# Kernel tuning notes

Measured on AMD Instinct MI355X. Metric: run time of the kernel, lower is better.

Reference implementation:

```python
import jax, jax.numpy as jnp
import numpy as np

# Topologies derived from init kwargs (inputs=64, outputs=64, state=512, net1 hidden=[512])
D = 64 + 64 + 512                      # 640 = concat(input, prev_output, state)
NET1 = [D, 512, 64]
NET3 = [D] + NET1 + [512]              # [640, 640, 512, 64, 512] (code reuses mutated net1 topo)
W_TOTAL = sum(NET3[j] * NET3[j + 1] for j in range(len(NET3) - 1))  # 802816
B_TOTAL = sum(NET3[1:])                # 1728
NET2 = [D] + NET1 + [W_TOTAL + B_TOTAL]  # [640, 640, 512, 64, 804544]


def _leaky(v):
    return jnp.where(v >= 0, v, 0.01 * v)


def setup_inputs() -> dict:
    key = jax.random.key(0)
    ks = jax.random.split(key, 16)
    inp = {
        "x": jax.random.normal(ks[0], (64,), jnp.float32),
        "prev_output": jnp.zeros((64,), jnp.float32),
        "state": jnp.zeros((512,), jnp.float32),
    }
    # net1 params (Linear stores W as [out, in])
    for i in range(len(NET1) - 1):
        inp[f"net1_w{i}"] = jax.random.normal(ks[1 + i], (NET1[i + 1], NET1[i]), jnp.float32) * 0.02
        inp[f"net1_b{i}"] = jnp.zeros((NET1[i + 1],), jnp.float32)
    # net2 params
    for i in range(len(NET2) - 1):
        inp[f"net2_w{i}"] = jax.random.normal(ks[5 + i], (NET2[i + 1], NET2[i]), jnp.float32) * 0.02
        inp[f"net2_b{i}"] = jnp.zeros((NET2[i + 1],), jnp.float32)
    return inp


def reference(x, prev_output, state,
              net1_w0, net1_b0, net1_w1, net1_b1,
              net2_w0, net2_b0, net2_w1, net2_b1,
              net2_w2, net2_b2, net2_w3, net2_b3):
    inpt = jnp.concatenate([x, prev_output, state])  # [640]

    # net2: hypernetwork producing flattened weights+biases for net3
    h = _leaky(net2_w0 @ inpt + net2_b0)
    h = _leaky(net2_w1 @ h + net2_b1)
    h = _leaky(net2_w2 @ h + net2_b2)
    x2 = jnp.tanh(net2_w3 @ h + net2_b3) * 0.5       # [W_TOTAL + B_TOTAL]
    weights = x2[:W_TOTAL]
    bias = x2[W_TOTAL:]

    # net3: apply generated weights sequentially (state update)
    x3 = inpt
    wi, bi = 0, 0
    for j in range(1, len(NET3)):
        out_d, in_d = NET3[j], NET3[j - 1]
        W = weights[wi:wi + out_d * in_d].reshape(out_d, in_d)
        b = bias[bi:bi + out_d]
        x3 = W @ x3 + b                               # 1D: x3 @ W.T == W @ x3
        if j != len(NET3) - 1:
            x3 = _leaky(x3)
        wi += out_d * in_d
        bi += out_d
    new_state = x3                                    # [512]

    # net1: output head
    h1 = _leaky(net1_w0 @ inpt + net1_b0)
    out = net1_w1 @ h1 + net1_b1                      # [64]

    # torch forward returns only `out`; new_state is the persistent buffer
    # update. We concatenate both so the full step math is observable.
    return jnp.concatenate([out, new_state])          # [576]
```

## Files before the change

kernel.cpp:

```cpp
#include <hip/hip_runtime.h>
#include <math.h>


#define WS_H0    0
#define WS_H1N1  640
#define WS_H1N2  1152
#define WS_H2    1664
#define WS_INPT  1728
#define WS_X3A   2368
#define WS_X3B   3008
#define WS_X3C   3520

__device__ __forceinline__ float leaky_f(float v) { return v >= 0.0f ? v : 0.01f * v; }

__device__ __forceinline__ float inpt_at(int i, const float* x, const float* po, const float* st) {
  return i < 64 ? x[i] : (i < 128 ? po[i - 64] : st[i - 128]);
}

__device__ __forceinline__ float half_tanh(float d) {
  float t = exp2f(d * 2.8853900817779268f);
  return 0.5f - __builtin_amdgcn_rcpf(t + 1.0f);
}

template <int IN>
__device__ __forceinline__ float row_dot(const float* __restrict__ wrow, const float* s_in, int lane) {
  const float4* w4 = (const float4*)wrow;
  const float4* s4 = (const float4*)s_in;
  float acc = 0.f;
  for (int j = lane; j < IN / 4; j += 64) {
    float4 a = w4[j];
    float4 b = s4[j];
    acc += a.x * b.x + a.y * b.y + a.z * b.z + a.w * b.w;
  }
  for (int off = 32; off; off >>= 1) acc += __shfl_xor(acc, off, 64);
  return acc;
}

__global__ __launch_bounds__(256) void k1a(const float* __restrict__ x, const float* __restrict__ po,
                                           const float* __restrict__ st,
                                           const float* __restrict__ w2_0, const float* __restrict__ b2_0,
                                           const float* __restrict__ w1_0, const float* __restrict__ b1_0,
                                           float* __restrict__ ws) {
  __shared__ __align__(16) float s_in[640];
  for (int i = threadIdx.x; i < 640; i += 256) {
    float v = inpt_at(i, x, po, st);
    s_in[i] = v;
    ws[WS_INPT + i] = v;
  }
  __syncthreads();
  int wave = threadIdx.x >> 6, lane = threadIdx.x & 63;
  int o = blockIdx.x * 4 + wave;
  const float* wrow;
  float bias;
  float* dst;
  if (o < 640) {
    wrow = w2_0 + (long long)o * 640; bias = b2_0[o]; dst = ws + WS_H0 + o;
  } else {
    int oo = o - 640;
    wrow = w1_0 + (long long)oo * 640; bias = b1_0[oo]; dst = ws + WS_H1N1 + oo;
  }
  float acc = row_dot<640>(wrow, s_in, lane);
  if (lane == 0) *dst = leaky_f(acc + bias);
}

__global__ __launch_bounds__(256) void k1b(const float* __restrict__ w2_1, const float* __restrict__ b2_1,
                                           const float* __restrict__ w1_1, const float* __restrict__ b1_1,
                                           float* __restrict__ ws, float* __restrict__ out) {
  __shared__ __align__(16) float s_h0[640];
  __shared__ __align__(16) float s_h1[512];
  for (int i = threadIdx.x; i < 640; i += 256) s_h0[i] = ws[WS_H0 + i];
  for (int i = threadIdx.x; i < 512; i += 256) s_h1[i] = ws[WS_H1N1 + i];
  __syncthreads();
  int wave = threadIdx.x >> 6, lane = threadIdx.x & 63;
  int o = blockIdx.x * 4 + wave;
  if (o < 512) {
    float acc = row_dot<640>(w2_1 + (long long)o * 640, s_h0, lane);
    if (lane == 0) ws[WS_H1N2 + o] = leaky_f(acc + b2_1[o]);
  } else {
    int oo = o - 512;
    float acc = row_dot<512>(w1_1 + (long long)oo * 512, s_h1, lane);
    if (lane == 0) out[oo] = acc + b1_1[oo];
  }
}

__global__ __launch_bounds__(256) void k1c(const float* __restrict__ w2_2, const float* __restrict__ b2_2,
                                           float* __restrict__ ws) {
  __shared__ __align__(16) float s_h[512];
  for (int i = threadIdx.x; i < 512; i += 256) s_h[i] = ws[WS_H1N2 + i];
  __syncthreads();
  int wave = threadIdx.x >> 6, lane = threadIdx.x & 63;
  int o = blockIdx.x * 4 + wave;
  float acc = row_dot<512>(w2_2 + (long long)o * 512, s_h, lane);
  if (lane == 0) ws[WS_H2 + o] = leaky_f(acc + b2_2[o]);
}

template <int IN_D, bool LEAKY>
__global__ __launch_bounds__(512) void k2c(const float* __restrict__ w3, const float* __restrict__ b3,
                                           const float* __restrict__ h2p, const float* __restrict__ x3in,
                                           float* __restrict__ x3out, long long wi, long long brow) {
  __shared__ __align__(16) float s_in[IN_D];
  __shared__ float s_red[8];
  const int tid = threadIdx.x;
  const int wave = tid >> 6, lane = tid & 63;
  const int g = lane >> 4;
  const int gl = lane & 15;

  float4 hv = ((const float4*)h2p)[gl];
  for (int i = tid; i < IN_D; i += 512) s_in[i] = x3in[i];
  __syncthreads();

  const int o = blockIdx.x;
  const long long rowbase = wi + (long long)o * IN_D;
  float acc = 0.0f;
  constexpr int STEPS = IN_D / 32;
#pragma unroll
  for (int s = 0; s < STEPS; s++) {
    int rl = s * 32 + wave * 4 + g;
    long long r = rowbase + rl;
    float4 v = ((const float4*)(w3 + (r << 6)))[gl];
    float d = v.x * hv.x + v.y * hv.y + v.z * hv.z + v.w * hv.w;
    d += __shfl_xor(d, 1, 64);
    d += __shfl_xor(d, 2, 64);
    d += __shfl_xor(d, 4, 64);
    d += __shfl_xor(d, 8, 64);
    d += b3[r];
    float x2v = half_tanh(d);
    if (gl == 0) acc += x2v * s_in[rl];
  }
  if (wave == 0 && lane < 16) {
    long long rb = brow + o;
    float4 v = ((const float4*)(w3 + (rb << 6)))[gl];
    float d = v.x * hv.x + v.y * hv.y + v.z * hv.z + v.w * hv.w;
    d += __shfl_xor(d, 1, 64);
    d += __shfl_xor(d, 2, 64);
    d += __shfl_xor(d, 4, 64);
    d += __shfl_xor(d, 8, 64);
    d += b3[rb];
    if (lane == 0) acc += half_tanh(d);
  }
  for (int off = 32; off; off >>= 1) acc += __shfl_xor(acc, off, 64);
  if (lane == 0) s_red[wave] = acc;
  __syncthreads();
  if (tid == 0) {
    float tot = 0.f;
#pragma unroll
    for (int w = 0; w < 8; w++) tot += s_red[w];
    x3out[o] = LEAKY ? leaky_f(tot) : tot;
  }
}

extern "C" void kernel_launch(void* const* d_in, const int* in_sizes, int n_in,
                              void* d_out, int out_size, void* d_ws, size_t ws_size,
                              hipStream_t stream) {
  const float* x    = (const float*)d_in[0];
  const float* po   = (const float*)d_in[1];
  const float* st   = (const float*)d_in[2];
  const float* w1_0 = (const float*)d_in[3];
  const float* b1_0 = (const float*)d_in[4];
  const float* w1_1 = (const float*)d_in[5];
  const float* b1_1 = (const float*)d_in[6];
  const float* w2_0 = (const float*)d_in[7];
  const float* b2_0 = (const float*)d_in[8];
  const float* w2_1 = (const float*)d_in[9];
  const float* b2_1 = (const float*)d_in[10];
  const float* w2_2 = (const float*)d_in[11];
  const float* b2_2 = (const float*)d_in[12];
  const float* w3   = (const float*)d_in[13];
  const float* b3   = (const float*)d_in[14];
  float* ws  = (float*)d_ws;
  float* out = (float*)d_out;

  k1a<<<288, 256, 0, stream>>>(x, po, st, w2_0, b2_0, w1_0, b1_0, ws);
  k1b<<<144, 256, 0, stream>>>(w2_1, b2_1, w1_1, b1_1, ws, out);
  k1c<<<16, 256, 0, stream>>>(w2_2, b2_2, ws);
  k2c<640, true><<<640, 512, 0, stream>>>(w3, b3, ws + WS_H2, ws + WS_INPT, ws + WS_X3A, 0LL, 802816LL);
  k2c<640, true><<<512, 512, 0, stream>>>(w3, b3, ws + WS_H2, ws + WS_X3A, ws + WS_X3B, 409600LL, 803456LL);
  k2c<512, true><<<64, 512, 0, stream>>>(w3, b3, ws + WS_H2, ws + WS_X3B, ws + WS_X3C, 737280LL, 803968LL);
  k2c<64, false><<<512, 512, 0, stream>>>(w3, b3, ws + WS_H2, ws + WS_X3C, out + 64, 770048LL, 804032LL);
}
```

Before: 355.6 us.

## Compute all hypernetwork outputs in one wide kernel, then run net3 matvecs

Replaces the four sequential fused k2c launches with a single bigT kernel that computes every tanh output of net2's last layer (weights and biases for net3) into a workspace buffer. Small gml matvec kernels then apply the generated weights layer by layer. The point is to expose the full 206 MB weight stream to the whole GPU at once instead of serialising it across dependent layers with poorly occupied grids such as 64 blocks. Each wave preloads 16 float4 registers for memory-level parallelism. The cost is an extra write and read of a roughly 3.2 MB intermediate and more launches.

```diff
diff --git a/kernel.cpp b/kernel.cpp
--- a/kernel.cpp
+++ b/kernel.cpp
@@ -10,6 +10,10 @@
 #define WS_X3A   2368
 #define WS_X3B   3008
 #define WS_X3C   3520
+#define WS_T     4096
+
+#define N_ROWS   804544
+#define N_WAVES  12571
 
 __device__ __forceinline__ float leaky_f(float v) { return v >= 0.0f ? v : 0.01f * v; }
 
@@ -94,58 +98,47 @@
   if (lane == 0) ws[WS_H2 + o] = leaky_f(acc + b2_2[o]);
 }
 
-template <int IN_D, bool LEAKY>
-__global__ __launch_bounds__(512) void k2c(const float* __restrict__ w3, const float* __restrict__ b3,
-                                           const float* __restrict__ h2p, const float* __restrict__ x3in,
-                                           float* __restrict__ x3out, long long wi, long long brow) {
-  __shared__ __align__(16) float s_in[IN_D];
-  __shared__ float s_red[8];
-  const int tid = threadIdx.x;
-  const int wave = tid >> 6, lane = tid & 63;
+__global__ __launch_bounds__(256) void bigT(const float* __restrict__ w3, const float* __restrict__ b3,
+                                            const float* __restrict__ h2p, float* __restrict__ t) {
+  int wid = blockIdx.x * 4 + (threadIdx.x >> 6);
+  if (wid >= N_WAVES) return;
+  const int lane = threadIdx.x & 63;
   const int g = lane >> 4;
   const int gl = lane & 15;
-
   float4 hv = ((const float4*)h2p)[gl];
-  for (int i = tid; i < IN_D; i += 512) s_in[i] = x3in[i];
-  __syncthreads();
-
-  const int o = blockIdx.x;
-  const long long rowbase = wi + (long long)o * IN_D;
-  float acc = 0.0f;
-  constexpr int STEPS = IN_D / 32;
+  const long long base = (long long)wid * 64;
+  const float4* wp = (const float4*)(w3 + (base << 6));
+  float4 v[16];
 #pragma unroll
-  for (int s = 0; s < STEPS; s++) {
-    int rl = s * 32 + wave * 4 + g;
-    long long r = rowbase + rl;
-    float4 v = ((const float4*)(w3 + (r << 6)))[gl];
-    float d = v.x * hv.x + v.y * hv.y + v.z * hv.z + v.w * hv.w;
+  for (int q = 0; q < 16; q++) v[q] = wp[((q * 4 + g) << 4) + gl];
+#pragma unroll
+  for (int q = 0; q < 16; q++) {
+    float d = v[q].x * hv.x + v[q].y * hv.y + v[q].z * hv.z + v[q].w * hv.w;
     d += __shfl_xor(d, 1, 64);
     d += __shfl_xor(d, 2, 64);
     d += __shfl_xor(d, 4, 64);
     d += __shfl_xor(d, 8, 64);
-    d += b3[r];
-    float x2v = half_tanh(d);
-    if (gl == 0) acc += x2v * s_in[rl];
+    if (gl == 0) {
+      long long r = base + q * 4 + g;
+      t[r] = half_tanh(d + b3[r]);
+    }
   }
-  if (wave == 0 && lane < 16) {
-    long long rb = brow + o;
-    float4 v = ((const float4*)(w3 + (rb << 6)))[gl];
-    float d = v.x * hv.x + v.y * hv.y + v.z * hv.z + v.w * hv.w;
-    d += __shfl_xor(d, 1, 64);
-    d += __shfl_xor(d, 2, 64);
-    d += __shfl_xor(d, 4, 64);
-    d += __shfl_xor(d, 8, 64);
-    d += b3[rb];
-    if (lane == 0) acc += half_tanh(d);
-  }
-  for (int off = 32; off; off >>= 1) acc += __shfl_xor(acc, off, 64);
-  if (lane == 0) s_red[wave] = acc;
+}
+
+template <int IN, bool LEAKY>
+__global__ __launch_bounds__(256) void gml(const float* __restrict__ t, const float* __restrict__ x3in,
+                                           float* __restrict__ x3out, long long wi, long long brow,
+                                           int OUT) {
+  __shared__ __align__(16) float s_in[IN];
+  for (int i = threadIdx.x; i < IN; i += 256) s_in[i] = x3in[i];
   __syncthreads();
-  if (tid == 0) {
-    float tot = 0.f;
-#pragma unroll
-    for (int w = 0; w < 8; w++) tot += s_red[w];
-    x3out[o] = LEAKY ? leaky_f(tot) : tot;
+  int wave = threadIdx.x >> 6, lane = threadIdx.x & 63;
+  int o = blockIdx.x * 4 + wave;
+  if (o >= OUT) return;
+  float acc = row_dot<IN>(t + wi + (long long)o * IN, s_in, lane);
+  if (lane == 0) {
+    acc += t[brow + o];
+    x3out[o] = LEAKY ? leaky_f(acc) : acc;
   }
 }
 
@@ -169,12 +162,14 @@
   const float* b3   = (const float*)d_in[14];
   float* ws  = (float*)d_ws;
   float* out = (float*)d_out;
+  float* t   = ws + WS_T;
 
   k1a<<<288, 256, 0, stream>>>(x, po, st, w2_0, b2_0, w1_0, b1_0, ws);
   k1b<<<144, 256, 0, stream>>>(w2_1, b2_1, w1_1, b1_1, ws, out);
   k1c<<<16, 256, 0, stream>>>(w2_2, b2_2, ws);
-  k2c<640, true><<<640, 512, 0, stream>>>(w3, b3, ws + WS_H2, ws + WS_INPT, ws + WS_X3A, 0LL, 802816LL);
-  k2c<640, true><<<512, 512, 0, stream>>>(w3, b3, ws + WS_H2, ws + WS_X3A, ws + WS_X3B, 409600LL, 803456LL);
-  k2c<512, true><<<64, 512, 0, stream>>>(w3, b3, ws + WS_H2, ws + WS_X3B, ws + WS_X3C, 737280LL, 803968LL);
-  k2c<64, false><<<512, 512, 0, stream>>>(w3, b3, ws + WS_H2, ws + WS_X3C, out + 64, 770048LL, 804032LL);
+  bigT<<<(N_WAVES + 3) / 4, 256, 0, stream>>>(w3, b3, ws + WS_H2, t);
+  gml<640, true><<<160, 256, 0, stream>>>(t, ws + WS_INPT, ws + WS_X3A, 0LL, 802816LL, 640);
+  gml<640, true><<<128, 256, 0, stream>>>(t, ws + WS_X3A, ws + WS_X3B, 409600LL, 803456LL, 512);
+  gml<512, true><<<16, 256, 0, stream>>>(t, ws + WS_X3B, ws + WS_X3C, 737280LL, 803968LL, 64);
+  gml<64, false><<<128, 256, 0, stream>>>(t, ws + WS_X3C, out + 64, 770048LL, 804032LL, 512);
 }
```

Result: faster. 340.0 us (-4.4%).
